# Kernel optimization log

Measured on AMD Instinct MI355X. Metric: run time of the kernel, lower is better.

## Reference

```python
import jax, jax.numpy as jnp
import numpy as np

HID = 256      # cfg.MODEL.YOSO.HIDDEN_DIM
NPROP = 100    # cfg.MODEL.YOSO.NUM_PROPOSALS
K1 = 3         # CONV_KERNEL_SIZE_1D
K2 = 1         # CONV_KERNEL_SIZE_2D
NCLS = 80      # NUM_CLASSES
NHEAD = 8

def layernorm(x, g, b, eps=1e-5):
    m = jnp.mean(x, -1, keepdims=True)
    v = jnp.var(x, -1, keepdims=True)
    return (x - m) * jax.lax.rsqrt(v + eps) * g + b

def dysep(query, value, Wl, bl, ng, nb):
    # dynamic depthwise conv (kernel K1 along feature axis, one kernel per proposal)
    # followed by dynamic pointwise NxN conv, per torch F.conv1d semantics (cross-correlation, 'same' pad)
    w = query @ Wl + bl                      # [B,N,N+K1]
    dw = w[..., :K1]                         # [B,N,K1] depthwise kernels
    pw = w[..., K1:]                         # [B,N,N]  pointwise mixing
    C = value.shape[-1]
    pad = K1 // 2
    vp = jnp.pad(value, ((0, 0), (0, 0), (pad, pad)))
    depth = sum(dw[..., k:k + 1] * vp[..., k:k + C] for k in range(K1))
    depth = jax.nn.relu(depth)
    point = jnp.einsum('bmn,bnc->bmc', pw, depth)
    return layernorm(point, ng, nb)

def mha(x, in_w, in_b, out_w, out_b):
    B, N, E = x.shape
    d = E // NHEAD
    qkv = x @ in_w + in_b
    q, k, v = jnp.split(qkv, 3, axis=-1)
    q = q.reshape(B, N, NHEAD, d)
    k = k.reshape(B, N, NHEAD, d)
    v = v.reshape(B, N, NHEAD, d)
    att = jnp.einsum('bqhd,bkhd->bhqk', q, k) / jnp.sqrt(jnp.asarray(d, x.dtype))
    att = jax.nn.softmax(att, axis=-1)
    o = jnp.einsum('bhqk,bkhd->bqhd', att, v).reshape(B, N, E)
    return o @ out_w + out_b

def setup_inputs() -> dict:
    key = jax.random.key(0)
    ks = iter(jax.random.split(key, 64))
    B, H, W = 8, 128, 128
    E = HID * K2 * K2
    nrm = lambda *s: jax.random.normal(next(ks), s, jnp.float32) * 0.02
    bias_value = -np.log((1 - 0.01) / 0.01)
    return dict(
        features=jax.random.normal(next(ks), (B, HID, H, W), jnp.float32),
        proposal_kernels=jax.random.normal(next(ks), (B, NPROP, E), jnp.float32),
        mask_preds=jax.random.normal(next(ks), (B, NPROP, H, W), jnp.float32),
        fW=nrm(E, NPROP + K1), fb=jnp.zeros(NPROP + K1), fng=jnp.ones(E), fnb=jnp.zeros(E),
        f_norm_g=jnp.ones(E), f_norm_b=jnp.zeros(E),
        kW=nrm(E, NPROP + K1), kb=jnp.zeros(NPROP + K1), kng=jnp.ones(E), knb=jnp.zeros(E),
        k_norm_g=jnp.ones(E), k_norm_b=jnp.zeros(E),
        attn_in_w=nrm(E, 3 * E), attn_in_b=jnp.zeros(3 * E),
        attn_out_w=nrm(E, E), attn_out_b=jnp.zeros(E),
        s_norm_g=jnp.ones(E), s_norm_b=jnp.zeros(E),
        ffn_w1=nrm(HID, 2048), ffn_b1=jnp.zeros(2048),
        ffn_w2=nrm(2048, HID), ffn_b2=jnp.zeros(HID),
        ffn_norm_g=jnp.ones(HID), ffn_norm_b=jnp.zeros(HID),
        cls_w=nrm(HID, HID), cls_ln_g=jnp.ones(HID), cls_ln_b=jnp.zeros(HID),
        fc_cls_w=nrm(HID, NCLS + 1), fc_cls_b=jnp.full((NCLS + 1,), bias_value, jnp.float32),
        mask_w=nrm(3, HID, HID), mask_ln_g=jnp.ones((3, HID)), mask_ln_b=jnp.zeros((3, HID)),
        fc_mask_w=nrm(HID, HID), fc_mask_b=jnp.zeros(HID),
        train_flag=1,
    )

def reference(features, proposal_kernels, mask_preds, fW, fb, fng, fnb, f_norm_g, f_norm_b,
              kW, kb, kng, knb, k_norm_g, k_norm_b,
              attn_in_w, attn_in_b, attn_out_w, attn_out_b, s_norm_g, s_norm_b,
              ffn_w1, ffn_b1, ffn_w2, ffn_b2, ffn_norm_g, ffn_norm_b,
              cls_w, cls_ln_g, cls_ln_b, fc_cls_w, fc_cls_b,
              mask_w, mask_ln_g, mask_ln_b, fc_mask_w, fc_mask_b, train_flag):
    B, C, H, W = features.shape
    hard = (jax.nn.sigmoid(mask_preds) > 0.5).astype(features.dtype)   # hard masks (no grad path)
    f = jnp.einsum('bnhw,bchw->bnc', hard, features)                   # mask-pooled features [B,N,E]
    k = proposal_kernels.reshape(B, NPROP, -1)
    f = layernorm(f + dysep(k, f, fW, fb, fng, fnb), f_norm_g, f_norm_b)
    kk = layernorm(f + dysep(k, f, kW, kb, kng, knb), k_norm_g, k_norm_b)
    kk = layernorm(kk + mha(kk, attn_in_w, attn_in_b, attn_out_w, attn_out_b), s_norm_g, s_norm_b)
    obj = jnp.transpose(kk.reshape(B, NPROP, HID, -1), (0, 1, 3, 2))   # [B,N,K2*K2,HID]
    h = jax.nn.relu(obj @ ffn_w1 + ffn_b1)
    obj = layernorm(obj + (h @ ffn_w2 + ffn_b2), ffn_norm_g, ffn_norm_b)
    cls_feat = obj.sum(-2)                                             # [B,N,HID]
    mask_feat = obj
    if train_flag:
        cls_feat = jax.nn.relu(layernorm(cls_feat @ cls_w, cls_ln_g, cls_ln_b))
        cls_score = (cls_feat @ fc_cls_w + fc_cls_b).reshape(B, NPROP, -1)
    else:
        cls_score = None
    for i in range(mask_w.shape[0]):
        mask_feat = jax.nn.relu(layernorm(mask_feat @ mask_w[i], mask_ln_g[i], mask_ln_b[i]))
    mask_kernels = (mask_feat @ fc_mask_w + fc_mask_b)[:, :, 0, :]     # squeeze(2), K2*K2==1
    new_mask_preds = jnp.einsum('bqc,bchw->bqhw', mask_kernels, features)
    obj_out = jnp.transpose(obj, (0, 1, 3, 2)).reshape(B, NPROP, HID, K2, K2)
    return (cls_score, new_mask_preds, obj_out)
```

## Files before the change

### kernel.cpp

```cpp
#include <hip/hip_runtime.h>

typedef float f32x4 __attribute__((ext_vector_type(4)));
typedef short bfrag __attribute__((ext_vector_type(8)));
typedef short sh4 __attribute__((ext_vector_type(4)));

__device__ __forceinline__ unsigned short f2bf(float x) {
  unsigned int u = __float_as_uint(x);
  return (unsigned short)((u + 0x7FFFu + ((u >> 16) & 1u)) >> 16);
}
__device__ __forceinline__ float bf2f(unsigned short u) {
  return __uint_as_float(((unsigned int)u) << 16);
}
__device__ __forceinline__ float wred_sum(float v) {
#pragma unroll
  for (int o = 32; o > 0; o >>= 1) v += __shfl_xor(v, o);
  return v;
}
__device__ __forceinline__ float wred_max(float v) {
#pragma unroll
  for (int o = 32; o > 0; o >>= 1) v = fmaxf(v, __shfl_xor(v, o));
  return v;
}

struct Prep12 {
  const float* s[12];
  int K[12];
  int N[12];
  int base[12];
  int doff[12];
};

__global__ __launch_bounds__(256) void prep_w(Prep12 p, unsigned short* wt) {
  int t = blockIdx.x;
  int wi = 0;
#pragma unroll
  for (int i = 0; i < 11; ++i)
    if (t >= p.base[i + 1]) wi = i + 1;
  int lt = t - p.base[wi];
  int K = p.K[wi], N = p.N[wi];
  int tkn = (K + 31) >> 5;
  int tk = lt % tkn, tn = lt / tkn;
  __shared__ float tile[32][33];
  const float* src = p.s[wi];
#pragma unroll
  for (int i = 0; i < 4; ++i) {
    int flat = i * 256 + threadIdx.x;
    int kl = flat >> 5, nl = flat & 31;
    int k = tk * 32 + kl, n = tn * 32 + nl;
    tile[kl][nl] = (k < K && n < N) ? src[(size_t)k * N + n] : 0.f;
  }
  __syncthreads();
  unsigned short* dst = wt + p.doff[wi];
#pragma unroll
  for (int i = 0; i < 4; ++i) {
    int flat = i * 256 + threadIdx.x;
    int nl = flat >> 5, kl = flat & 31;
    int k = tk * 32 + kl, n = tn * 32 + nl;
    if (k < K && n < N) {
      int np = (wi < 2) ? ((n >= 3) ? n - 3 : n + 100) : n;
      dst[(size_t)np * K + k] = f2bf(tile[kl][nl]);
    }
  }
}

__global__ __launch_bounds__(256) void prep_bias(const float* __restrict__ fb_,
                                                 const float* __restrict__ kb_,
                                                 float* __restrict__ bf,
                                                 float* __restrict__ bk) {
  int t = threadIdx.x;
  if (t < 103) {
    int np = (t >= 3) ? t - 3 : t + 100;
    bf[np] = fb_[t];
    bk[np] = kb_[t];
  }
  if (t == 103) { bf[103] = 0.f; bk[103] = 0.f; }
}

template <int ABF, int OBF>
__global__ __launch_bounds__(256) void gemm_mf(const void* Av,
                                               const unsigned short* __restrict__ Wt,
                                               const float* __restrict__ bias,
                                               void* Cv, int M, int K, int N, int ldc, int relu) {
  __shared__ short Al[64 * 72];
  __shared__ short Wl[64 * 72];
  int tid = threadIdx.x;
  int r0 = blockIdx.x * 64;
  int c0 = blockIdx.y * 64;
  int w = tid >> 6, lane = tid & 63, quad = lane >> 4, l15 = lane & 15;

  f32x4 acc[4];
#pragma unroll
  for (int mt = 0; mt < 4; ++mt) {
    acc[mt][0] = 0.f; acc[mt][1] = 0.f; acc[mt][2] = 0.f; acc[mt][3] = 0.f;
  }

  for (int k0 = 0; k0 < K; k0 += 64) {
    if (ABF) {
      const unsigned short* A = (const unsigned short*)Av;
#pragma unroll
      for (int p = 0; p < 2; ++p) {
        int flat = p * 256 + tid;
        int row = flat >> 3, k8 = flat & 7;
        bfrag v;
        if (r0 + row < M)
          v = *(const bfrag*)(A + (size_t)(r0 + row) * K + k0 + k8 * 8);
        else
          v = (bfrag)(short)0;
        *(bfrag*)(Al + row * 72 + k8 * 8) = v;
      }
    } else {
      const float* A = (const float*)Av;
#pragma unroll
      for (int p = 0; p < 4; ++p) {
        int flat = p * 256 + tid;
        int row = flat >> 4, c4 = flat & 15;
        sh4 o4;
        if (r0 + row < M) {
          float4 v = *(const float4*)(A + (size_t)(r0 + row) * K + k0 + c4 * 4);
          o4[0] = (short)f2bf(v.x); o4[1] = (short)f2bf(v.y);
          o4[2] = (short)f2bf(v.z); o4[3] = (short)f2bf(v.w);
        } else {
          o4[0] = 0; o4[1] = 0; o4[2] = 0; o4[3] = 0;
        }
        *(sh4*)(Al + row * 72 + c4 * 4) = o4;
      }
    }
#pragma unroll
    for (int p = 0; p < 2; ++p) {
      int flat = p * 256 + tid;
      int row = flat >> 3, k8 = flat & 7;
      bfrag v;
      if (c0 + row < N)
        v = *(const bfrag*)(Wt + (size_t)(c0 + row) * K + k0 + k8 * 8);
      else
        v = (bfrag)(short)0;
      *(bfrag*)(Wl + row * 72 + k8 * 8) = v;
    }
    __syncthreads();
#pragma unroll
    for (int kk = 0; kk < 2; ++kk) {
      bfrag bv = *(const bfrag*)(Wl + (w * 16 + l15) * 72 + kk * 32 + quad * 8);
#pragma unroll
      for (int mt = 0; mt < 4; ++mt) {
        bfrag av = *(const bfrag*)(Al + (mt * 16 + l15) * 72 + kk * 32 + quad * 8);
        acc[mt] = __builtin_amdgcn_mfma_f32_16x16x32_bf16(av, bv, acc[mt], 0, 0, 0);
      }
    }
    __syncthreads();
  }
  int col = c0 + w * 16 + l15;
  if (col < N) {
    float bv = bias ? bias[col] : 0.f;
#pragma unroll
    for (int mt = 0; mt < 4; ++mt)
#pragma unroll
      for (int r = 0; r < 4; ++r) {
        int m = r0 + mt * 16 + quad * 4 + r;
        if (m < M) {
          float v = acc[mt][r] + bv;
          if (relu) v = fmaxf(v, 0.f);
          if (OBF)
            ((unsigned short*)Cv)[(size_t)m * ldc + col] = f2bf(v);
          else
            ((float*)Cv)[(size_t)m * ldc + col] = v;
        }
      }
  }
}

__global__ __launch_bounds__(512, 4) void phaseA(const float* __restrict__ mask,
                                                 const float* __restrict__ feat,
                                                 float* __restrict__ partial) {
  int tid = threadIdx.x;
  int ks = blockIdx.x;
  int ct = blockIdx.y;
  int b  = blockIdx.z;
  __shared__ short Al[2][112 * 72];
  __shared__ short Bl[2][128 * 72];
  int w = tid >> 6, lane = tid & 63, quad = lane >> 4, l15 = lane & 15;

  int rbase = tid >> 4;
  int c4 = tid & 15;
  const float* mrow = mask + (size_t)(b * 100 + rbase) * 16384 + c4 * 4;
  const float* frow = feat + (size_t)(b * 256 + ct * 128 + rbase) * 16384 + c4 * 4;

  f32x4 acc[7];
#pragma unroll
  for (int mt = 0; mt < 7; ++mt) {
    acc[mt][0] = 0.f; acc[mt][1] = 0.f; acc[mt][2] = 0.f; acc[mt][3] = 0.f;
  }

  for (int z = tid; z < 384; z += 512) {
    int bufi = z / 192, rem = z % 192;
    sh4 zz; zz[0] = 0; zz[1] = 0; zz[2] = 0; zz[3] = 0;
    *(sh4*)(&Al[bufi][(100 + (rem >> 4)) * 72 + (rem & 15) * 4]) = zz;
  }

  int k0 = ks * 512;
  {
    float4 apf[4], bpf[4];
#pragma unroll
    for (int p = 0; p < 4; ++p) {
      int row = rbase + 32 * p;
      if (row < 100) apf[p] = *(const float4*)(mrow + (size_t)p * 32 * 16384 + k0);
      bpf[p] = *(const float4*)(frow + (size_t)p * 32 * 16384 + k0);
    }
#pragma unroll
    for (int p = 0; p < 4; ++p) {
      int row = rbase + 32 * p;
      if (row < 100) {
        sh4 o4;
        o4[0] = (apf[p].x > 0.f) ? (short)0x3F80 : (short)0;
        o4[1] = (apf[p].y > 0.f) ? (short)0x3F80 : (short)0;
        o4[2] = (apf[p].z > 0.f) ? (short)0x3F80 : (short)0;
        o4[3] = (apf[p].w > 0.f) ? (short)0x3F80 : (short)0;
        *(sh4*)(&Al[0][row * 72 + c4 * 4]) = o4;
      }
      sh4 o4b;
      o4b[0] = (short)f2bf(bpf[p].x);
      o4b[1] = (short)f2bf(bpf[p].y);
      o4b[2] = (short)f2bf(bpf[p].z);
      o4b[3] = (short)f2bf(bpf[p].w);
      *(sh4*)(&Bl[0][row * 72 + c4 * 4]) = o4b;
    }
  }
  __syncthreads();

  int cur = 0;
  for (int st = 0; st < 8; ++st) {
    float4 apf[4], bpf[4];
    if (st < 7) {
      int kb = k0 + (st + 1) * 64;
#pragma unroll
      for (int p = 0; p < 4; ++p) {
        int row = rbase + 32 * p;
        if (row < 100) apf[p] = *(const float4*)(mrow + (size_t)p * 32 * 16384 + kb);
        bpf[p] = *(const float4*)(frow + (size_t)p * 32 * 16384 + kb);
      }
    }
#pragma unroll
    for (int kk = 0; kk < 2; ++kk) {
      bfrag bv = *(const bfrag*)(&Bl[cur][(w * 16 + l15) * 72 + kk * 32 + quad * 8]);
#pragma unroll
      for (int mt = 0; mt < 7; ++mt) {
        bfrag av = *(const bfrag*)(&Al[cur][(mt * 16 + l15) * 72 + kk * 32 + quad * 8]);
        acc[mt] = __builtin_amdgcn_mfma_f32_16x16x32_bf16(av, bv, acc[mt], 0, 0, 0);
      }
    }
    __builtin_amdgcn_sched_barrier(0);
    if (st < 7) {
      int nxt = cur ^ 1;
#pragma unroll
      for (int p = 0; p < 4; ++p) {
        int row = rbase + 32 * p;
        if (row < 100) {
          sh4 o4;
          o4[0] = (apf[p].x > 0.f) ? (short)0x3F80 : (short)0;
          o4[1] = (apf[p].y > 0.f) ? (short)0x3F80 : (short)0;
          o4[2] = (apf[p].z > 0.f) ? (short)0x3F80 : (short)0;
          o4[3] = (apf[p].w > 0.f) ? (short)0x3F80 : (short)0;
          *(sh4*)(&Al[nxt][row * 72 + c4 * 4]) = o4;
        }
        sh4 o4b;
        o4b[0] = (short)f2bf(bpf[p].x);
        o4b[1] = (short)f2bf(bpf[p].y);
        o4b[2] = (short)f2bf(bpf[p].z);
        o4b[3] = (short)f2bf(bpf[p].w);
        *(sh4*)(&Bl[nxt][row * 72 + c4 * 4]) = o4b;
      }
    }
    __syncthreads();
    cur ^= 1;
  }

  float* pb = partial + (size_t)(b * 32 + ks) * (100 * 256) + ct * 128 + w * 16 + l15;
#pragma unroll
  for (int mt = 0; mt < 7; ++mt)
#pragma unroll
    for (int r = 0; r < 4; ++r) {
      int m = mt * 16 + quad * 4 + r;
      if (m < 100) pb[(size_t)m * 256] = acc[mt][r];
    }
}

__global__ __launch_bounds__(256) void reduceA(const float* __restrict__ partial,
                                               float* __restrict__ fm) {
  int gid = blockIdx.x * 256 + threadIdx.x;
  int c = gid & 255, row = gid >> 8;
  int b = row / 100, n = row % 100;
  float s = 0.f;
#pragma unroll
  for (int ks = 0; ks < 32; ++ks)
    s += partial[((size_t)(b * 32 + ks) * 100 + n) * 256 + c];
  fm[(size_t)row * 256 + c] = s;
}

__global__ __launch_bounds__(256) void pointdw(const float* __restrict__ fm,
                                               const float* __restrict__ wbuf,
                                               float* __restrict__ point) {
  int tid = threadIdx.x;
  int b = blockIdx.y, c0 = blockIdx.x * 32;
  __shared__ float dl[100 * 33];
  for (int flat = tid; flat < 3200; flat += 256) {
    int n = flat >> 5, cl = flat & 31, c = c0 + cl;
    const float* fr = fm + (size_t)(b * 100 + n) * 256;
    const float* wr = wbuf + (size_t)(b * 100 + n) * 104;
    float x0 = (c > 0) ? fr[c - 1] : 0.f;
    float x1 = fr[c];
    float x2 = (c < 255) ? fr[c + 1] : 0.f;
    float d = wr[100] * x0 + wr[101] * x1 + wr[102] * x2;
    dl[n * 33 + cl] = fmaxf(d, 0.f);
  }
  __syncthreads();
  int cl = tid & 31, mg = tid >> 5;
  for (int m = mg; m < 100; m += 8) {
    const float4* pw4 = (const float4*)(wbuf + (size_t)(b * 100 + m) * 104);
    float a = 0.f;
#pragma unroll
    for (int n4 = 0; n4 < 25; ++n4) {
      float4 wv = pw4[n4];
      a += wv.x * dl[(n4 * 4 + 0) * 33 + cl] + wv.y * dl[(n4 * 4 + 1) * 33 + cl]
         + wv.z * dl[(n4 * 4 + 2) * 33 + cl] + wv.w * dl[(n4 * 4 + 3) * 33 + cl];
    }
    point[(size_t)(b * 100 + m) * 256 + c0 + cl] = a;
  }
}

__global__ __launch_bounds__(256) void ln2_kernel(const float* __restrict__ x,
                                                  const float* __restrict__ resid,
                                                  const float* __restrict__ g1, const float* __restrict__ b1,
                                                  const float* __restrict__ g2, const float* __restrict__ b2,
                                                  float* __restrict__ out) {
  int tid = threadIdx.x;
  int row = blockIdx.x * 4 + (tid >> 6);
  int lane = tid & 63;
  size_t base = (size_t)row * 256 + lane * 4;
  float4 v = *(const float4*)(x + base);
  float mean = wred_sum(v.x + v.y + v.z + v.w) * (1.f / 256.f);
  float d0 = v.x - mean, d1 = v.y - mean, d2 = v.z - mean, d3 = v.w - mean;
  float rs = rsqrtf(wred_sum(d0 * d0 + d1 * d1 + d2 * d2 + d3 * d3) * (1.f / 256.f) + 1e-5f);
  float4 gv = *(const float4*)(g1 + lane * 4);
  float4 bv = *(const float4*)(b1 + lane * 4);
  float4 rv = *(const float4*)(resid + base);
  float y0 = rv.x + d0 * rs * gv.x + bv.x;
  float y1 = rv.y + d1 * rs * gv.y + bv.y;
  float y2 = rv.z + d2 * rs * gv.z + bv.z;
  float y3 = rv.w + d3 * rs * gv.w + bv.w;
  float mean2 = wred_sum(y0 + y1 + y2 + y3) * (1.f / 256.f);
  float e0 = y0 - mean2, e1 = y1 - mean2, e2 = y2 - mean2, e3 = y3 - mean2;
  float rs2 = rsqrtf(wred_sum(e0 * e0 + e1 * e1 + e2 * e2 + e3 * e3) * (1.f / 256.f) + 1e-5f);
  float4 g2v = *(const float4*)(g2 + lane * 4);
  float4 b2v = *(const float4*)(b2 + lane * 4);
  float4 o;
  o.x = e0 * rs2 * g2v.x + b2v.x;
  o.y = e1 * rs2 * g2v.y + b2v.y;
  o.z = e2 * rs2 * g2v.z + b2v.z;
  o.w = e3 * rs2 * g2v.w + b2v.w;
  *(float4*)(out + base) = o;
}

__global__ __launch_bounds__(256) void ln_kernel(const float* __restrict__ x,
                                                 const float* __restrict__ res,
                                                 const float* __restrict__ g, const float* __restrict__ bb,
                                                 float* __restrict__ out, int relu,
                                                 float* __restrict__ copy2) {
  int tid = threadIdx.x;
  int row = blockIdx.x * 4 + (tid >> 6);
  int lane = tid & 63;
  size_t base = (size_t)row * 256 + lane * 4;
  float4 v = *(const float4*)(x + base);
  if (res) {
    float4 rv = *(const float4*)(res + base);
    v.x += rv.x; v.y += rv.y; v.z += rv.z; v.w += rv.w;
  }
  float mean = wred_sum(v.x + v.y + v.z + v.w) * (1.f / 256.f);
  float d0 = v.x - mean, d1 = v.y - mean, d2 = v.z - mean, d3 = v.w - mean;
  float rs = rsqrtf(wred_sum(d0 * d0 + d1 * d1 + d2 * d2 + d3 * d3) * (1.f / 256.f) + 1e-5f);
  float4 gv = *(const float4*)(g + lane * 4);
  float4 bv = *(const float4*)(bb + lane * 4);
  float4 o;
  o.x = d0 * rs * gv.x + bv.x;
  o.y = d1 * rs * gv.y + bv.y;
  o.z = d2 * rs * gv.z + bv.z;
  o.w = d3 * rs * gv.w + bv.w;
  if (relu) {
    o.x = fmaxf(o.x, 0.f); o.y = fmaxf(o.y, 0.f);
    o.z = fmaxf(o.z, 0.f); o.w = fmaxf(o.w, 0.f);
  }
  *(float4*)(out + base) = o;
  if (copy2) *(float4*)(copy2 + base) = o;
}

__global__ __launch_bounds__(256) void attn_kernel(const float* __restrict__ qkv,
                                                   float* __restrict__ obuf) {
  int tid = threadIdx.x;
  int b = blockIdx.y, h = blockIdx.x;
  __shared__ float ktj[100 * 32];
  __shared__ unsigned short vl[100 * 32];
  __shared__ float sl[100 * 100];
  const float* base = qkv + (size_t)b * 100 * 768;
  for (int flat = tid; flat < 3200; flat += 256) {
    int j = flat >> 5, dd = flat & 31;
    ktj[j * 32 + dd] = base[(size_t)j * 768 + 256 + h * 32 + dd];
    vl[j * 32 + dd] = f2bf(base[(size_t)j * 768 + 512 + h * 32 + dd]);
  }
  __syncthreads();
  {
    int i = tid >> 1;
    int jh = (tid & 1) * 50;
    int qi = (i < 100) ? i : 0;
    const float4* q4 = (const float4*)(base + (size_t)qi * 768 + h * 32);
    float4 q[8];
#pragma unroll
    for (int d4 = 0; d4 < 8; ++d4) q[d4] = q4[d4];
    if (i < 100) {
      for (int jj = 0; jj < 50; ++jj) {
        int j = jh + jj;
        const float4* kr = (const float4*)(ktj + j * 32);
        float a = 0.f;
#pragma unroll
        for (int d4 = 0; d4 < 8; ++d4) {
          float4 kv = kr[d4];
          a += q[d4].x * kv.x + q[d4].y * kv.y + q[d4].z * kv.z + q[d4].w * kv.w;
        }
        sl[i * 100 + j] = a * 0.17677669529663687f;
      }
    }
  }
  __syncthreads();
  int w = tid >> 6, lane = tid & 63;
  for (int r = w; r < 100; r += 4) {
    float x0 = sl[r * 100 + lane];
    float x1 = (lane + 64 < 100) ? sl[r * 100 + lane + 64] : -1e30f;
    float mx = wred_max(fmaxf(x0, x1));
    float e0 = __expf(x0 - mx);
    float e1 = (lane + 64 < 100) ? __expf(x1 - mx) : 0.f;
    float inv = 1.f / wred_sum(e0 + e1);
    sl[r * 100 + lane] = e0 * inv;
    if (lane + 64 < 100) sl[r * 100 + lane + 64] = e1 * inv;
  }
  __syncthreads();
  for (int flat = tid; flat < 3200; flat += 256) {
    int i = flat >> 5, dd = flat & 31;
    float a = 0.f;
#pragma unroll 4
    for (int j = 0; j < 100; ++j) a += sl[i * 100 + j] * bf2f(vl[j * 32 + dd]);
    obuf[(size_t)(b * 100 + i) * 256 + h * 32 + dd] = a;
  }
}

__global__ __launch_bounds__(256) void phaseE(const float* __restrict__ mk,
                                              const float* __restrict__ feat,
                                              float* __restrict__ out) {
  int tid = threadIdx.x;
  int b = blockIdx.y;
  int hw0 = blockIdx.x * 128;
  __shared__ short Al[112 * 264];
#pragma unroll
  for (int p = 0; p < 28; ++p) {
    int flat = p * 256 + tid;
    int row = flat >> 6, c4 = flat & 63;
    sh4 o4;
    if (row < 100) {
      float4 v = *(const float4*)(mk + (size_t)(b * 100 + row) * 256 + c4 * 4);
      o4[0] = (short)f2bf(v.x); o4[1] = (short)f2bf(v.y);
      o4[2] = (short)f2bf(v.z); o4[3] = (short)f2bf(v.w);
    } else {
      o4[0] = 0; o4[1] = 0; o4[2] = 0; o4[3] = 0;
    }
    *(sh4*)(Al + row * 264 + c4 * 4) = o4;
  }
  __syncthreads();
  int w = tid >> 6, lane = tid & 63, quad = lane >> 4, l15 = lane & 15;
  f32x4 acc[7][2];
#pragma unroll
  for (int mt = 0; mt < 7; ++mt)
#pragma unroll
    for (int nt = 0; nt < 2; ++nt) {
      acc[mt][nt][0] = 0.f; acc[mt][nt][1] = 0.f; acc[mt][nt][2] = 0.f; acc[mt][nt][3] = 0.f;
    }
  size_t fb = (size_t)b * 256 * 16384;
  int hwl = hw0 + w * 32 + l15;
  for (int kk = 0; kk < 8; ++kk) {
    bfrag bv[2];
#pragma unroll
    for (int nt = 0; nt < 2; ++nt) {
#pragma unroll
      for (int j = 0; j < 8; ++j) {
        float v = feat[fb + (size_t)(kk * 32 + quad * 8 + j) * 16384 + hwl + nt * 16];
        bv[nt][j] = (short)f2bf(v);
      }
    }
    bfrag av[7];
#pragma unroll
    for (int mt = 0; mt < 7; ++mt)
      av[mt] = *(const bfrag*)(Al + (mt * 16 + l15) * 264 + kk * 32 + quad * 8);
#pragma unroll
    for (int mt = 0; mt < 7; ++mt) {
      acc[mt][0] = __builtin_amdgcn_mfma_f32_16x16x32_bf16(av[mt], bv[0], acc[mt][0], 0, 0, 0);
      acc[mt][1] = __builtin_amdgcn_mfma_f32_16x16x32_bf16(av[mt], bv[1], acc[mt][1], 0, 0, 0);
    }
  }
#pragma unroll
  for (int mt = 0; mt < 7; ++mt)
#pragma unroll
    for (int nt = 0; nt < 2; ++nt)
#pragma unroll
      for (int r = 0; r < 4; ++r) {
        int m = mt * 16 + quad * 4 + r;
        if (m < 100)
          out[(size_t)(b * 100 + m) * 16384 + hw0 + w * 32 + nt * 16 + l15] = acc[mt][nt][r];
      }
}

extern "C" void kernel_launch(void* const* d_in, const int* in_sizes, int n_in,
                              void* d_out, int out_size, void* d_ws, size_t ws_size,
                              hipStream_t stream) {
  const float* feat    = (const float*)d_in[0];
  const float* prop    = (const float*)d_in[1];
  const float* maskp   = (const float*)d_in[2];
  const float* fW      = (const float*)d_in[3];
  const float* fb_     = (const float*)d_in[4];
  const float* fng     = (const float*)d_in[5];
  const float* fnb     = (const float*)d_in[6];
  const float* f_ng    = (const float*)d_in[7];
  const float* f_nb    = (const float*)d_in[8];
  const float* kW      = (const float*)d_in[9];
  const float* kb_     = (const float*)d_in[10];
  const float* kng     = (const float*)d_in[11];
  const float* knb     = (const float*)d_in[12];
  const float* k_ng    = (const float*)d_in[13];
  const float* k_nb    = (const float*)d_in[14];
  const float* aw_in   = (const float*)d_in[15];
  const float* ab_in   = (const float*)d_in[16];
  const float* aw_out  = (const float*)d_in[17];
  const float* ab_out  = (const float*)d_in[18];
  const float* s_ng    = (const float*)d_in[19];
  const float* s_nb    = (const float*)d_in[20];
  const float* w1      = (const float*)d_in[21];
  const float* b1      = (const float*)d_in[22];
  const float* w2      = (const float*)d_in[23];
  const float* b2      = (const float*)d_in[24];
  const float* ffn_ng  = (const float*)d_in[25];
  const float* ffn_nb  = (const float*)d_in[26];
  const float* cls_w   = (const float*)d_in[27];
  const float* cls_g   = (const float*)d_in[28];
  const float* cls_b   = (const float*)d_in[29];
  const float* fcclsw  = (const float*)d_in[30];
  const float* fcclsb  = (const float*)d_in[31];
  const float* mask_w  = (const float*)d_in[32];
  const float* mask_g  = (const float*)d_in[33];
  const float* mask_b  = (const float*)d_in[34];
  const float* fcmw    = (const float*)d_in[35];
  const float* fcmb    = (const float*)d_in[36];
  float* out = (float*)d_out;

  float* ws = (float*)d_ws;
  size_t off = 0;
  unsigned short* wt = (unsigned short*)(ws + off); off += 856192;
  float* fm     = ws + off; off += 204800;
  float* bias_f = ws + off; off += 104;
  float* bias_k = ws + off; off += 104;
  float* partial = ws + off;
  float* ub = partial;
  size_t uo = 0;
  float* wb   = ub + uo; uo += 83200;
  float* pt   = ub + uo; uo += 204800;
  float* fbuf = ub + uo; uo += 204800;
  float* kkb  = ub + uo; uo += 204800;
  float* qkvb = ub + uo; uo += 614400;
  float* ob   = ub + uo; uo += 204800;
  float* mo   = ub + uo; uo += 204800;
  float* kk2  = ub + uo; uo += 204800;
  float* t1   = ub + uo; uo += 204800;
  float* objb = ub + uo; uo += 204800;
  float* t2   = ub + uo; uo += 204800;
  float* mkb  = ub + uo; uo += 204800;
  unsigned short* ffn1b = (unsigned short*)(ub + uo); uo += 409600;

  const int wt_fW = 0, wt_kW = 26624, wt_ain = 53248, wt_aout = 249856;
  const int wt_w1 = 315392, wt_w2 = 839680, wt_cls = 1363968, wt_fccls = 1429504;
  const int wt_m0 = 1450240, wt_m1 = 1515776, wt_m2 = 1581312, wt_fcm = 1646848;

  float* out_cls  = out;
  float* out_mask = out + 64800;
  float* out_obj  = out + 64800 + 13107200;

  Prep12 p;
  const float* srcs[12] = {fW, kW, aw_in, aw_out, w1, w2, cls_w, fcclsw,
                           mask_w, mask_w + 65536, mask_w + 131072, fcmw};
  int Ks[12]    = {256, 256, 256, 256, 256, 2048, 256, 256, 256, 256, 256, 256};
  int Ns[12]    = {103, 103, 768, 256, 2048, 256, 256, 81, 256, 256, 256, 256};
  int doffs[12] = {wt_fW, wt_kW, wt_ain, wt_aout, wt_w1, wt_w2, wt_cls, wt_fccls,
                   wt_m0, wt_m1, wt_m2, wt_fcm};
  int tb = 0;
  for (int i = 0; i < 12; ++i) {
    p.s[i] = srcs[i]; p.K[i] = Ks[i]; p.N[i] = Ns[i]; p.doff[i] = doffs[i];
    p.base[i] = tb;
    tb += ((Ks[i] + 31) / 32) * ((Ns[i] + 31) / 32);
  }
  prep_w<<<tb, 256, 0, stream>>>(p, wt);
  prep_bias<<<1, 256, 0, stream>>>(fb_, kb_, bias_f, bias_k);

  phaseA<<<dim3(32, 2, 8), 512, 0, stream>>>(maskp, feat, partial);
  reduceA<<<800, 256, 0, stream>>>(partial, fm);
  gemm_mf<0, 0><<<dim3(13, 2), 256, 0, stream>>>(prop, wt + wt_fW, bias_f, wb, 800, 256, 103, 104, 0);
  pointdw<<<dim3(8, 8), 256, 0, stream>>>(fm, wb, pt);
  ln2_kernel<<<200, 256, 0, stream>>>(pt, fm, fng, fnb, f_ng, f_nb, fbuf);
  gemm_mf<0, 0><<<dim3(13, 2), 256, 0, stream>>>(prop, wt + wt_kW, bias_k, wb, 800, 256, 103, 104, 0);
  pointdw<<<dim3(8, 8), 256, 0, stream>>>(fbuf, wb, pt);
  ln2_kernel<<<200, 256, 0, stream>>>(pt, fbuf, kng, knb, k_ng, k_nb, kkb);
  gemm_mf<0, 0><<<dim3(13, 12), 256, 0, stream>>>(kkb, wt + wt_ain, ab_in, qkvb, 800, 256, 768, 768, 0);
  attn_kernel<<<dim3(8, 8), 256, 0, stream>>>(qkvb, ob);
  gemm_mf<0, 0><<<dim3(13, 4), 256, 0, stream>>>(ob, wt + wt_aout, ab_out, mo, 800, 256, 256, 256, 0);
  ln_kernel<<<200, 256, 0, stream>>>(mo, kkb, s_ng, s_nb, kk2, 0, nullptr);
  gemm_mf<0, 1><<<dim3(13, 32), 256, 0, stream>>>(kk2, wt + wt_w1, b1, ffn1b, 800, 256, 2048, 2048, 1);
  gemm_mf<1, 0><<<dim3(13, 4), 256, 0, stream>>>(ffn1b, wt + wt_w2, b2, t1, 800, 2048, 256, 256, 0);
  ln_kernel<<<200, 256, 0, stream>>>(t1, kk2, ffn_ng, ffn_nb, objb, 0, out_obj);
  gemm_mf<0, 0><<<dim3(13, 4), 256, 0, stream>>>(objb, wt + wt_cls, nullptr, t1, 800, 256, 256, 256, 0);
  ln_kernel<<<200, 256, 0, stream>>>(t1, nullptr, cls_g, cls_b, t2, 1, nullptr);
  gemm_mf<0, 0><<<dim3(13, 2), 256, 0, stream>>>(t2, wt + wt_fccls, fcclsb, out_cls, 800, 256, 81, 81, 0);
  gemm_mf<0, 0><<<dim3(13, 4), 256, 0, stream>>>(objb, wt + wt_m0, nullptr, t1, 800, 256, 256, 256, 0);
  ln_kernel<<<200, 256, 0, stream>>>(t1, nullptr, mask_g, mask_b, t2, 1, nullptr);
  gemm_mf<0, 0><<<dim3(13, 4), 256, 0, stream>>>(t2, wt + wt_m1, nullptr, t1, 800, 256, 256, 256, 0);
  ln_kernel<<<200, 256, 0, stream>>>(t1, nullptr, mask_g + 256, mask_b + 256, t2, 1, nullptr);
  gemm_mf<0, 0><<<dim3(13, 4), 256, 0, stream>>>(t2, wt + wt_m2, nullptr, t1, 800, 256, 256, 256, 0);
  ln_kernel<<<200, 256, 0, stream>>>(t1, nullptr, mask_g + 512, mask_b + 512, t2, 1, nullptr);
  gemm_mf<0, 0><<<dim3(13, 4), 256, 0, stream>>>(t2, wt + wt_fcm, fcmb, mkb, 800, 256, 256, 256, 0);
  phaseE<<<dim3(128, 8), 256, 0, stream>>>(mkb, feat, out_mask);
}
```

Baseline: 680.5 us.

## Single-buffer phaseA LDS for occupancy; feed phaseE bf16 mask kernels directly from global

phaseA drops its double-buffered LDS staging and register prefetch in favour of a simple load-sync-compute loop with a single buffer. The launch bound is raised to request twice the occupancy, so other waves are meant to hide load latency instead of software pipelining. Separately, the final mask GEMM now writes bf16 output, and phaseE reads its A fragments straight from global memory instead of converting them through LDS. This removes the LDS staging and a sync in phaseE, at the cost of redundant global reads per block and less explicit overlap in phaseA.

```diff
diff --git a/kernel.cpp b/kernel.cpp
--- a/kernel.cpp
+++ b/kernel.cpp
@@ -168,15 +168,15 @@
   }
 }
 
-__global__ __launch_bounds__(512, 4) void phaseA(const float* __restrict__ mask,
+__global__ __launch_bounds__(512, 8) void phaseA(const float* __restrict__ mask,
                                                  const float* __restrict__ feat,
                                                  float* __restrict__ partial) {
   int tid = threadIdx.x;
   int ks = blockIdx.x;
   int ct = blockIdx.y;
   int b  = blockIdx.z;
-  __shared__ short Al[2][112 * 72];
-  __shared__ short Bl[2][128 * 72];
+  __shared__ short Al[112 * 72];
+  __shared__ short Bl[128 * 72];
   int w = tid >> 6, lane = tid & 63, quad = lane >> 4, l15 = lane & 15;
 
   int rbase = tid >> 4;
@@ -190,20 +190,20 @@
     acc[mt][0] = 0.f; acc[mt][1] = 0.f; acc[mt][2] = 0.f; acc[mt][3] = 0.f;
   }
 
-  for (int z = tid; z < 384; z += 512) {
-    int bufi = z / 192, rem = z % 192;
+  for (int z = tid; z < 192; z += 512) {
     sh4 zz; zz[0] = 0; zz[1] = 0; zz[2] = 0; zz[3] = 0;
-    *(sh4*)(&Al[bufi][(100 + (rem >> 4)) * 72 + (rem & 15) * 4]) = zz;
+    *(sh4*)(&Al[(100 + (z >> 4)) * 72 + (z & 15) * 4]) = zz;
   }
 
   int k0 = ks * 512;
-  {
+  for (int st = 0; st < 8; ++st) {
+    int kb = k0 + st * 64;
     float4 apf[4], bpf[4];
 #pragma unroll
     for (int p = 0; p < 4; ++p) {
       int row = rbase + 32 * p;
-      if (row < 100) apf[p] = *(const float4*)(mrow + (size_t)p * 32 * 16384 + k0);
-      bpf[p] = *(const float4*)(frow + (size_t)p * 32 * 16384 + k0);
+      if (row < 100) apf[p] = *(const float4*)(mrow + (size_t)p * 32 * 16384 + kb);
+      bpf[p] = *(const float4*)(frow + (size_t)p * 32 * 16384 + kb);
     }
 #pragma unroll
     for (int p = 0; p < 4; ++p) {
@@ -214,63 +214,26 @@
         o4[1] = (apf[p].y > 0.f) ? (short)0x3F80 : (short)0;
         o4[2] = (apf[p].z > 0.f) ? (short)0x3F80 : (short)0;
         o4[3] = (apf[p].w > 0.f) ? (short)0x3F80 : (short)0;
-        *(sh4*)(&Al[0][row * 72 + c4 * 4]) = o4;
+        *(sh4*)(&Al[row * 72 + c4 * 4]) = o4;
       }
       sh4 o4b;
       o4b[0] = (short)f2bf(bpf[p].x);
       o4b[1] = (short)f2bf(bpf[p].y);
       o4b[2] = (short)f2bf(bpf[p].z);
       o4b[3] = (short)f2bf(bpf[p].w);
-      *(sh4*)(&Bl[0][row * 72 + c4 * 4]) = o4b;
-    }
-  }
-  __syncthreads();
-
-  int cur = 0;
-  for (int st = 0; st < 8; ++st) {
-    float4 apf[4], bpf[4];
-    if (st < 7) {
-      int kb = k0 + (st + 1) * 64;
-#pragma unroll
-      for (int p = 0; p < 4; ++p) {
-        int row = rbase + 32 * p;
-        if (row < 100) apf[p] = *(const float4*)(mrow + (size_t)p * 32 * 16384 + kb);
-        bpf[p] = *(const float4*)(frow + (size_t)p * 32 * 16384 + kb);
-      }
-    }
+      *(sh4*)(&Bl[row * 72 + c4 * 4]) = o4b;
+    }
+    __syncthreads();
 #pragma unroll
     for (int kk = 0; kk < 2; ++kk) {
-      bfrag bv = *(const bfrag*)(&Bl[cur][(w * 16 + l15) * 72 + kk * 32 + quad * 8]);
+      bfrag bv = *(const bfrag*)(&Bl[(w * 16 + l15) * 72 + kk * 32 + quad * 8]);
 #pragma unroll
       for (int mt = 0; mt < 7; ++mt) {
-        bfrag av = *(const bfrag*)(&Al[cur][(mt * 16 + l15) * 72 + kk * 32 + quad * 8]);
+        bfrag av = *(const bfrag*)(&Al[(mt * 16 + l15) * 72 + kk * 32 + quad * 8]);
         acc[mt] = __builtin_amdgcn_mfma_f32_16x16x32_bf16(av, bv, acc[mt], 0, 0, 0);
       }
     }
-    __builtin_amdgcn_sched_barrier(0);
-    if (st < 7) {
-      int nxt = cur ^ 1;
-#pragma unroll
-      for (int p = 0; p < 4; ++p) {
-        int row = rbase + 32 * p;
-        if (row < 100) {
-          sh4 o4;
-          o4[0] = (apf[p].x > 0.f) ? (short)0x3F80 : (short)0;
-          o4[1] = (apf[p].y > 0.f) ? (short)0x3F80 : (short)0;
-          o4[2] = (apf[p].z > 0.f) ? (short)0x3F80 : (short)0;
-          o4[3] = (apf[p].w > 0.f) ? (short)0x3F80 : (short)0;
-          *(sh4*)(&Al[nxt][row * 72 + c4 * 4]) = o4;
-        }
-        sh4 o4b;
-        o4b[0] = (short)f2bf(bpf[p].x);
-        o4b[1] = (short)f2bf(bpf[p].y);
-        o4b[2] = (short)f2bf(bpf[p].z);
-        o4b[3] = (short)f2bf(bpf[p].w);
-        *(sh4*)(&Bl[nxt][row * 72 + c4 * 4]) = o4b;
-      }
-    }
     __syncthreads();
-    cur ^= 1;
   }
 
   float* pb = partial + (size_t)(b * 32 + ks) * (100 * 256) + ct * 128 + w * 16 + l15;
@@ -449,28 +412,12 @@
   }
 }
 
-__global__ __launch_bounds__(256) void phaseE(const float* __restrict__ mk,
-                                              const float* __restrict__ feat,
-                                              float* __restrict__ out) {
+__global__ __launch_bounds__(256, 4) void phaseE(const unsigned short* __restrict__ mk16,
+                                                 const float* __restrict__ feat,
+                                                 float* __restrict__ out) {
   int tid = threadIdx.x;
   int b = blockIdx.y;
   int hw0 = blockIdx.x * 128;
-  __shared__ short Al[112 * 264];
-#pragma unroll
-  for (int p = 0; p < 28; ++p) {
-    int flat = p * 256 + tid;
-    int row = flat >> 6, c4 = flat & 63;
-    sh4 o4;
-    if (row < 100) {
-      float4 v = *(const float4*)(mk + (size_t)(b * 100 + row) * 256 + c4 * 4);
-      o4[0] = (short)f2bf(v.x); o4[1] = (short)f2bf(v.y);
-      o4[2] = (short)f2bf(v.z); o4[3] = (short)f2bf(v.w);
-    } else {
-      o4[0] = 0; o4[1] = 0; o4[2] = 0; o4[3] = 0;
-    }
-    *(sh4*)(Al + row * 264 + c4 * 4) = o4;
-  }
-  __syncthreads();
   int w = tid >> 6, lane = tid & 63, quad = lane >> 4, l15 = lane & 15;
   f32x4 acc[7][2];
 #pragma unroll
@@ -481,6 +428,7 @@
     }
   size_t fb = (size_t)b * 256 * 16384;
   int hwl = hw0 + w * 32 + l15;
+  const unsigned short* mkb_b = mk16 + (size_t)b * 100 * 256;
   for (int kk = 0; kk < 8; ++kk) {
     bfrag bv[2];
 #pragma unroll
@@ -493,8 +441,11 @@
     }
     bfrag av[7];
 #pragma unroll
-    for (int mt = 0; mt < 7; ++mt)
-      av[mt] = *(const bfrag*)(Al + (mt * 16 + l15) * 264 + kk * 32 + quad * 8);
+    for (int mt = 0; mt < 7; ++mt) {
+      int row = mt * 16 + l15;
+      int rr = (row < 100) ? row : 0;
+      av[mt] = *(const bfrag*)(mkb_b + (size_t)rr * 256 + kk * 32 + quad * 8);
+    }
 #pragma unroll
     for (int mt = 0; mt < 7; ++mt) {
       acc[mt][0] = __builtin_amdgcn_mfma_f32_16x16x32_bf16(av[mt], bv[0], acc[mt][0], 0, 0, 0);
@@ -577,6 +528,7 @@
   float* t2   = ub + uo; uo += 204800;
   float* mkb  = ub + uo; uo += 204800;
   unsigned short* ffn1b = (unsigned short*)(ub + uo); uo += 409600;
+  unsigned short* mkb16 = (unsigned short*)mkb;
 
   const int wt_fW = 0, wt_kW = 26624, wt_ain = 53248, wt_aout = 249856;
   const int wt_w1 = 315392, wt_w2 = 839680, wt_cls = 1363968, wt_fccls = 1429504;
@@ -626,6 +578,6 @@
   ln_kernel<<<200, 256, 0, stream>>>(t1, nullptr, mask_g + 256, mask_b + 256, t2, 1, nullptr);
   gemm_mf<0, 0><<<dim3(13, 4), 256, 0, stream>>>(t2, wt + wt_m2, nullptr, t1, 800, 256, 256, 256, 0);
   ln_kernel<<<200, 256, 0, stream>>>(t1, nullptr, mask_g + 512, mask_b + 512, t2, 1, nullptr);
-  gemm_mf<0, 0><<<dim3(13, 4), 256, 0, stream>>>(t2, wt + wt_fcm, fcmb, mkb, 800, 256, 256, 256, 0);
-  phaseE<<<dim3(128, 8), 256, 0, stream>>>(mkb, feat, out_mask);
-}
+  gemm_mf<0, 1><<<dim3(13, 4), 256, 0, stream>>>(t2, wt + wt_fcm, fcmb, mkb16, 800, 256, 256, 256, 0);
+  phaseE<<<dim3(128, 8), 256, 0, stream>>>(mkb16, feat, out_mask);
+}
```

Result: slower. 703.3 us (+3.4%).
